# Performance work log

Measured on AMD Instinct MI355X. Metric: run time of the kernel, lower is better.

Reference implementation:

```python
import jax, jax.numpy as jnp
import numpy as np

N = 50000
TOPK = 32
IN_C = 128
OUT_C = 64
NEG_SLOPE = 0.2
BN_EPS = 1e-5


def setup_inputs() -> dict:
    key = jax.random.key(0)
    ks = jax.random.split(key, 8)
    x = jax.random.normal(ks[0], (N, IN_C), dtype=jnp.float32)
    embedding = jax.random.normal(ks[1], (N, OUT_C), dtype=jnp.float32)
    # edges: each node has TOPK incoming edges, no self loops
    tgt = jnp.repeat(jnp.arange(N, dtype=jnp.int64), TOPK)
    off = jax.random.randint(ks[2], (N * TOPK,), 1, N, dtype=jnp.int64)
    src = (tgt + off) % N
    edge_index = jnp.stack([src, tgt], axis=0)
    lin_w = jax.random.normal(ks[3], (OUT_C, IN_C), dtype=jnp.float32) * (1.0 / np.sqrt(IN_C))
    att_i = jax.random.normal(ks[4], (1, 1, OUT_C), dtype=jnp.float32) * 0.1
    att_j = jax.random.normal(ks[5], (1, 1, OUT_C), dtype=jnp.float32) * 0.1
    att_em_i = jax.random.normal(ks[6], (1, 1, OUT_C), dtype=jnp.float32) * 0.1
    att_em_j = jax.random.normal(ks[7], (1, 1, OUT_C), dtype=jnp.float32) * 0.1
    bias = jnp.zeros((OUT_C,), dtype=jnp.float32)
    bn_gamma = jnp.ones((OUT_C,), dtype=jnp.float32)
    bn_beta = jnp.zeros((OUT_C,), dtype=jnp.float32)
    return {"x": x, "embedding": embedding, "edge_index": edge_index,
            "lin_w": lin_w, "att_i": att_i, "att_j": att_j,
            "att_em_i": att_em_i, "att_em_j": att_em_j, "bias": bias,
            "bn_gamma": bn_gamma, "bn_beta": bn_beta}


def _gnn_forward(x, embedding, lin_w, att_i, att_j, att_em_i, att_em_j,
                 bias, bn_gamma, bn_beta, src, tgt):
    n = x.shape[0]
    # linear transform: [N, heads=1, OUT_C]
    x_lin = (x @ lin_w.T).reshape(n, 1, OUT_C)
    # gather per edge (self loops already appended to src/tgt)
    x_i = x_lin[tgt]                      # [Etot, 1, C]
    x_j = x_lin[src]                      # [Etot, 1, C]
    emb_i = embedding[tgt][:, None, :]    # [Etot, 1, C]
    emb_j = embedding[src][:, None, :]
    # attention logits, eq (6)-(8)
    alpha = ((x_i * att_i).sum(-1) + (emb_i * att_em_i).sum(-1)
             + (x_j * att_j).sum(-1) + (emb_j * att_em_j).sum(-1))  # [Etot, 1]
    alpha = jnp.where(alpha >= 0, alpha, NEG_SLOPE * alpha)
    # segment softmax over incoming edges of each target node
    m = jax.ops.segment_max(alpha, tgt, num_segments=n)
    m = jnp.where(jnp.isfinite(m), m, 0.0)
    e = jnp.exp(alpha - m[tgt])
    denom = jax.ops.segment_sum(e, tgt, num_segments=n)
    alpha = e / (denom[tgt] + 1e-16)      # [Etot, 1]
    # weighted scatter-add aggregation
    msg = x_j * alpha[:, :, None]         # [Etot, 1, C]
    out = jax.ops.segment_sum(msg, tgt, num_segments=n).reshape(n, OUT_C)
    out = out + bias
    # BatchNorm1d (training-mode batch stats, biased var) + ReLU
    mu = out.mean(axis=0)
    var = ((out - mu) ** 2).mean(axis=0)
    out = (out - mu) / jnp.sqrt(var + BN_EPS) * bn_gamma + bn_beta
    return jax.nn.relu(out)


def reference(x, embedding, edge_index, lin_w, att_i, att_j, att_em_i,
              att_em_j, bias, bn_gamma, bn_beta):
    n = x.shape[0]
    loops = jnp.arange(n, dtype=edge_index.dtype)
    src = jnp.concatenate([edge_index[0], loops])
    tgt = jnp.concatenate([edge_index[1], loops])
    return _gnn_forward(x, embedding, lin_w, att_i, att_j, att_em_i,
                        att_em_j, bias, bn_gamma, bn_beta, src, tgt)
```

## Files before the change

kernel.cpp:

```cpp
#include <hip/hip_runtime.h>

#define NN 50000
#define TOPK 32
#define IN_C 128
#define OUT_C 64
#define NEG_SLOPE 0.2f
#define BN_EPS 1e-5f

#define K1_BLOCKS (NN / 16)
#define K2_BLOCKS (NN / 8)

#define WS_XBF   0
#define WS_AI    (NN * 32)
#define WS_AJ    (WS_AI + NN)
#define WS_SUMS  (WS_AJ + NN)

typedef __bf16 bf16x8 __attribute__((ext_vector_type(8)));
typedef float f32x4 __attribute__((ext_vector_type(4)));
union BF8 { unsigned short u[8]; bf16x8 v; };

__device__ inline float leaky(float a) { return a >= 0.f ? a : NEG_SLOPE * a; }
__device__ inline float bl(unsigned u) { return __uint_as_float(u << 16); }
__device__ inline float bh(unsigned u) { return __uint_as_float(u & 0xffff0000u); }

__device__ inline unsigned short f2bf(float f) {
    unsigned u = __float_as_uint(f);
    unsigned r = (u + 0x7fffu + ((u >> 16) & 1u)) >> 16;
    return (unsigned short)r;
}

__device__ inline void async16(const uint4* g, uint4* l) {
    __builtin_amdgcn_global_load_lds(
        (const __attribute__((address_space(1))) void*)(const void*)g,
        (__attribute__((address_space(3))) void*)(void*)l, 16, 0, 0);
}

__global__ __launch_bounds__(256) void k1_mfma(
    const float* __restrict__ x, const float* __restrict__ emb,
    const float* __restrict__ lin_w,
    const float* __restrict__ att_i, const float* __restrict__ att_j,
    const float* __restrict__ att_em_i, const float* __restrict__ att_em_j,
    unsigned short* __restrict__ x_bf, float* __restrict__ a_i,
    float* __restrict__ a_j, float* __restrict__ sums)
{
    __shared__ float redi[16][5], redj[16][5];
    __shared__ float eredi[16][17], eredj[16][17];
    const int tid = threadIdx.x;
    if (blockIdx.x == 0) {
#pragma unroll
        for (int i = 0; i < 4; ++i) sums[tid + i * 256] = 0.f;
    }

    const int lane = tid & 63;
    const int wv = tid >> 6;
    const int quad = lane >> 4;
    const int nn = lane & 15;
    const int base = blockIdx.x * 16;
    const int c = wv * 16 + nn;

    BF8 bfr[4], afr[4];
    {
        const float* wr = lin_w + (size_t)c * IN_C + quad * 8;
        const float* xr = x + (size_t)(base + nn) * IN_C + quad * 8;
#pragma unroll
        for (int s = 0; s < 4; ++s) {
            const float4 wa = *(const float4*)(wr + s * 32);
            const float4 wb = *(const float4*)(wr + s * 32 + 4);
            const float4 xa = *(const float4*)(xr + s * 32);
            const float4 xb = *(const float4*)(xr + s * 32 + 4);
            bfr[s].u[0] = f2bf(wa.x); bfr[s].u[1] = f2bf(wa.y);
            bfr[s].u[2] = f2bf(wa.z); bfr[s].u[3] = f2bf(wa.w);
            bfr[s].u[4] = f2bf(wb.x); bfr[s].u[5] = f2bf(wb.y);
            bfr[s].u[6] = f2bf(wb.z); bfr[s].u[7] = f2bf(wb.w);
            afr[s].u[0] = f2bf(xa.x); afr[s].u[1] = f2bf(xa.y);
            afr[s].u[2] = f2bf(xa.z); afr[s].u[3] = f2bf(xa.w);
            afr[s].u[4] = f2bf(xb.x); afr[s].u[5] = f2bf(xb.y);
            afr[s].u[6] = f2bf(xb.z); afr[s].u[7] = f2bf(xb.w);
        }
    }

    f32x4 acc = {0.f, 0.f, 0.f, 0.f};
#pragma unroll
    for (int s = 0; s < 4; ++s)
        acc = __builtin_amdgcn_mfma_f32_16x16x32_bf16(afr[s].v, bfr[s].v, acc,
                                                      0, 0, 0);

    const float aic = att_i[c], ajc = att_j[c];
    float pi[4], pj[4];
#pragma unroll
    for (int r = 0; r < 4; ++r) {
        const int node = base + quad * 4 + r;
        x_bf[(size_t)node * OUT_C + c] = f2bf(acc[r]);
        pi[r] = acc[r] * aic;
        pj[r] = acc[r] * ajc;
    }
#pragma unroll
    for (int d = 1; d < 16; d <<= 1) {
#pragma unroll
        for (int r = 0; r < 4; ++r) {
            pi[r] += __shfl_xor(pi[r], d, 64);
            pj[r] += __shfl_xor(pj[r], d, 64);
        }
    }
    if (nn == 0) {
#pragma unroll
        for (int r = 0; r < 4; ++r) {
            redi[quad * 4 + r][wv] = pi[r];
            redj[quad * 4 + r][wv] = pj[r];
        }
    }
    {
        const int nl = tid >> 4, c4 = tid & 15;
        const float4 e4 = ((const float4*)emb)[(size_t)(base + nl) * 16 + c4];
        const float4 i4 = ((const float4*)att_em_i)[c4];
        const float4 j4 = ((const float4*)att_em_j)[c4];
        eredi[nl][c4] = e4.x * i4.x + e4.y * i4.y + e4.z * i4.z + e4.w * i4.w;
        eredj[nl][c4] = e4.x * j4.x + e4.y * j4.y + e4.z * j4.z + e4.w * j4.w;
    }
    __syncthreads();
    if (tid < 16) {
        float si = redi[tid][0] + redi[tid][1] + redi[tid][2] + redi[tid][3];
        float sj = redj[tid][0] + redj[tid][1] + redj[tid][2] + redj[tid][3];
#pragma unroll
        for (int r = 0; r < 16; ++r) { si += eredi[tid][r]; sj += eredj[tid][r]; }
        a_i[base + tid] = si;
        a_j[base + tid] = sj;
    }
}

__global__ __launch_bounds__(64) void k2_attn(
    const int* __restrict__ src, const uint4* __restrict__ x_bf4,
    const float* __restrict__ a_j, const float* __restrict__ a_i,
    const float* __restrict__ bias, float* __restrict__ out,
    float* __restrict__ sums)
{
    __shared__ uint4 stage[33 * 64];
    __shared__ float wbuf[8][36];
    __shared__ float sb1[64][9], sb2[64][9];

    const int tid = threadIdx.x;
    const int g = tid >> 3;
    const int q = tid & 7;
    const int t = blockIdx.x * 8 + g;

    const int4* sp4 = (const int4*)(src + (size_t)t * TOPK);
    int4 s4[8];
#pragma unroll
    for (int i = 0; i < 8; ++i) s4[i] = sp4[i];
    const int4 sq = sp4[q];

#pragma unroll
    for (int i = 0; i < 8; ++i) {
        async16(x_bf4 + ((size_t)s4[i].x * 8 + q), &stage[(i * 4 + 0) * 64]);
        async16(x_bf4 + ((size_t)s4[i].y * 8 + q), &stage[(i * 4 + 1) * 64]);
        async16(x_bf4 + ((size_t)s4[i].z * 8 + q), &stage[(i * 4 + 2) * 64]);
        async16(x_bf4 + ((size_t)s4[i].w * 8 + q), &stage[(i * 4 + 3) * 64]);
    }
    async16(x_bf4 + ((size_t)t * 8 + q), &stage[32 * 64]);

    const float ai_t = a_i[t];
    float l0 = leaky(ai_t + a_j[sq.x]);
    float l1 = leaky(ai_t + a_j[sq.y]);
    float l2 = leaky(ai_t + a_j[sq.z]);
    float l3 = leaky(ai_t + a_j[sq.w]);
    const float ls = leaky(ai_t + a_j[t]);
    float mx = fmaxf(fmaxf(l0, l1), fmaxf(l2, l3));
#pragma unroll
    for (int d = 1; d < 8; d <<= 1) mx = fmaxf(mx, __shfl_xor(mx, d, 64));
    mx = fmaxf(mx, ls);
    const float e0 = __expf(l0 - mx), e1 = __expf(l1 - mx);
    const float e2 = __expf(l2 - mx), e3 = __expf(l3 - mx);
    const float es = __expf(ls - mx);
    float den = (e0 + e1) + (e2 + e3);
#pragma unroll
    for (int d = 1; d < 8; d <<= 1) den += __shfl_xor(den, d, 64);
    den += es + 1e-16f;
    const float inv = 1.f / den;

    ((float4*)&wbuf[g][q * 4])[0] =
        make_float4(e0 * inv, e1 * inv, e2 * inv, e3 * inv);
    if (q == 0) wbuf[g][32] = es * inv;
    __syncthreads();

    float4 w4[8];
#pragma unroll
    for (int i = 0; i < 8; ++i) w4[i] = ((const float4*)wbuf[g])[i];
    const float wself = wbuf[g][32];

    __builtin_amdgcn_s_waitcnt(0x0F70);
    __syncthreads();

    float A[8];
#pragma unroll
    for (int j = 0; j < 8; ++j) A[j] = 0.f;
#pragma unroll
    for (int e = 0; e < 33; ++e) {
        const uint4 u = stage[e * 64 + tid];
        const float w = (e < 32) ? ((const float*)&w4[e >> 2])[e & 3] : wself;
        A[0] = fmaf(w, bl(u.x), A[0]); A[1] = fmaf(w, bh(u.x), A[1]);
        A[2] = fmaf(w, bl(u.y), A[2]); A[3] = fmaf(w, bh(u.y), A[3]);
        A[4] = fmaf(w, bl(u.z), A[4]); A[5] = fmaf(w, bh(u.z), A[5]);
        A[6] = fmaf(w, bl(u.w), A[6]); A[7] = fmaf(w, bh(u.w), A[7]);
    }
    const float4 b0 = ((const float4*)bias)[q * 2];
    const float4 b1 = ((const float4*)bias)[q * 2 + 1];
    float v[8];
    v[0] = A[0] + b0.x; v[1] = A[1] + b0.y; v[2] = A[2] + b0.z; v[3] = A[3] + b0.w;
    v[4] = A[4] + b1.x; v[5] = A[5] + b1.y; v[6] = A[6] + b1.z; v[7] = A[7] + b1.w;
    float4* o4 = (float4*)(out + (size_t)t * OUT_C + q * 8);
    o4[0] = make_float4(v[0], v[1], v[2], v[3]);
    o4[1] = make_float4(v[4], v[5], v[6], v[7]);

#pragma unroll
    for (int j = 0; j < 8; ++j) {
        sb1[q * 8 + j][g] = v[j];
        sb2[q * 8 + j][g] = v[j] * v[j];
    }
    __syncthreads();
    {
        float t1 = 0.f, t2 = 0.f;
#pragma unroll
        for (int r = 0; r < 8; ++r) { t1 += sb1[tid][r]; t2 += sb2[tid][r]; }
        float* rep = sums + (blockIdx.x & 7) * 128;
        atomicAdd(&rep[tid], t1);
        atomicAdd(&rep[64 + tid], t2);
    }
}

__global__ __launch_bounds__(256) void k4_bn(
    float* __restrict__ out, const float* __restrict__ sums,
    const float* __restrict__ gamma, const float* __restrict__ beta)
{
    __shared__ float s_sc[64], s_sh[64];
    const int tid = threadIdx.x;
    if (tid < 64) {
        float s1 = 0.f, s2 = 0.f;
#pragma unroll
        for (int r = 0; r < 8; ++r) {
            s1 += sums[r * 128 + tid];
            s2 += sums[r * 128 + 64 + tid];
        }
        const float mu = s1 / (float)NN;
        const float ex2 = s2 / (float)NN;
        const float var = fmaxf(ex2 - mu * mu, 0.f);
        const float sc = gamma[tid] / sqrtf(var + BN_EPS);
        s_sc[tid] = sc;
        s_sh[tid] = beta[tid] - mu * sc;
    }
    __syncthreads();
    const int total = NN * OUT_C / 4;
    float4* p = (float4*)out;
    for (int idx = blockIdx.x * 256 + tid; idx < total; idx += gridDim.x * 256) {
        float4 v = p[idx];
        const int c0 = (idx & 15) * 4;
        v.x = fmaxf(fmaf(v.x, s_sc[c0 + 0], s_sh[c0 + 0]), 0.f);
        v.y = fmaxf(fmaf(v.y, s_sc[c0 + 1], s_sh[c0 + 1]), 0.f);
        v.z = fmaxf(fmaf(v.z, s_sc[c0 + 2], s_sh[c0 + 2]), 0.f);
        v.w = fmaxf(fmaf(v.w, s_sc[c0 + 3], s_sh[c0 + 3]), 0.f);
        p[idx] = v;
    }
}

extern "C" void kernel_launch(void* const* d_in, const int* in_sizes, int n_in,
                              void* d_out, int out_size, void* d_ws, size_t ws_size,
                              hipStream_t stream) {
    const float* x        = (const float*)d_in[0];
    const float* emb      = (const float*)d_in[1];
    const int*   edge     = (const int*)d_in[2];
    const float* lin_w    = (const float*)d_in[3];
    const float* att_i    = (const float*)d_in[4];
    const float* att_j    = (const float*)d_in[5];
    const float* att_em_i = (const float*)d_in[6];
    const float* att_em_j = (const float*)d_in[7];
    const float* bias     = (const float*)d_in[8];
    const float* gamma    = (const float*)d_in[9];
    const float* beta     = (const float*)d_in[10];

    float* ws    = (float*)d_ws;
    unsigned short* x_bf = (unsigned short*)(ws + WS_XBF);
    float* a_i   = ws + WS_AI;
    float* a_j   = ws + WS_AJ;
    float* sums  = ws + WS_SUMS;
    float* out   = (float*)d_out;

    k1_mfma<<<K1_BLOCKS, 256, 0, stream>>>(x, emb, lin_w, att_i, att_j,
                                           att_em_i, att_em_j, x_bf, a_i, a_j, sums);
    k2_attn<<<K2_BLOCKS, 64, 0, stream>>>(edge, (const uint4*)x_bf, a_j, a_i,
                                          bias, out, sums);
    k4_bn<<<1024, 256, 0, stream>>>(out, sums, gamma, beta);
}
```

Before: 163.4 us.

## Fold attention vectors into weight-projected vectors and drop LDS reductions in k1

Adds a one-block pre-kernel that computes lin_w^T·att_i and lin_w^T·att_j, so each node's attention logit becomes a direct fp32 dot product with the input row instead of a reduction over the MFMA output. In k1 this removes the shared-memory reduction arrays, the 16-wide shuffle reductions and the __syncthreads; one wave computes the logits with two shuffles. It also switches the bf16 conversion to native casts, adds an extra tiny kernel launch, and slightly changes numerics because the logits no longer go through the bf16 GEMM.

```diff
diff --git a/kernel.cpp b/kernel.cpp
--- a/kernel.cpp
+++ b/kernel.cpp
@@ -14,10 +14,11 @@
 #define WS_AI    (NN * 32)
 #define WS_AJ    (WS_AI + NN)
 #define WS_SUMS  (WS_AJ + NN)
+#define WS_WI    (WS_SUMS + 1024)
+#define WS_WJ    (WS_WI + 128)
 
 typedef __bf16 bf16x8 __attribute__((ext_vector_type(8)));
 typedef float f32x4 __attribute__((ext_vector_type(4)));
-union BF8 { unsigned short u[8]; bf16x8 v; };
 
 __device__ inline float leaky(float a) { return a >= 0.f ? a : NEG_SLOPE * a; }
 __device__ inline float bl(unsigned u) { return __uint_as_float(u << 16); }
@@ -28,6 +29,15 @@
     unsigned r = (u + 0x7fffu + ((u >> 16) & 1u)) >> 16;
     return (unsigned short)r;
 }
+__device__ inline bf16x8 cvt8(const float4 a, const float4 b) {
+    bf16x8 r;
+    r[0] = (__bf16)a.x; r[1] = (__bf16)a.y; r[2] = (__bf16)a.z; r[3] = (__bf16)a.w;
+    r[4] = (__bf16)b.x; r[5] = (__bf16)b.y; r[6] = (__bf16)b.z; r[7] = (__bf16)b.w;
+    return r;
+}
+__device__ inline float dot4(const float4 a, const float4 b) {
+    return fmaf(a.x, b.x, fmaf(a.y, b.y, fmaf(a.z, b.z, a.w * b.w)));
+}
 
 __device__ inline void async16(const uint4* g, uint4* l) {
     __builtin_amdgcn_global_load_lds(
@@ -35,22 +45,34 @@
         (__attribute__((address_space(3))) void*)(void*)l, 16, 0, 0);
 }
 
+__global__ __launch_bounds__(128) void k0_pre(
+    const float* __restrict__ lin_w, const float* __restrict__ att_i,
+    const float* __restrict__ att_j, float* __restrict__ wi,
+    float* __restrict__ wj, float* __restrict__ sums)
+{
+    const int k = threadIdx.x;
+    float si = 0.f, sj = 0.f;
+#pragma unroll 8
+    for (int c = 0; c < OUT_C; ++c) {
+        const float w = lin_w[c * IN_C + k];
+        si = fmaf(w, att_i[c], si);
+        sj = fmaf(w, att_j[c], sj);
+    }
+    wi[k] = si;
+    wj[k] = sj;
+#pragma unroll
+    for (int i = 0; i < 8; ++i) sums[k + i * 128] = 0.f;
+}
+
 __global__ __launch_bounds__(256) void k1_mfma(
     const float* __restrict__ x, const float* __restrict__ emb,
     const float* __restrict__ lin_w,
-    const float* __restrict__ att_i, const float* __restrict__ att_j,
+    const float* __restrict__ wi, const float* __restrict__ wj,
     const float* __restrict__ att_em_i, const float* __restrict__ att_em_j,
     unsigned short* __restrict__ x_bf, float* __restrict__ a_i,
-    float* __restrict__ a_j, float* __restrict__ sums)
-{
-    __shared__ float redi[16][5], redj[16][5];
-    __shared__ float eredi[16][17], eredj[16][17];
+    float* __restrict__ a_j)
+{
     const int tid = threadIdx.x;
-    if (blockIdx.x == 0) {
-#pragma unroll
-        for (int i = 0; i < 4; ++i) sums[tid + i * 256] = 0.f;
-    }
-
     const int lane = tid & 63;
     const int wv = tid >> 6;
     const int quad = lane >> 4;
@@ -58,74 +80,57 @@
     const int base = blockIdx.x * 16;
     const int c = wv * 16 + nn;
 
-    BF8 bfr[4], afr[4];
-    {
-        const float* wr = lin_w + (size_t)c * IN_C + quad * 8;
-        const float* xr = x + (size_t)(base + nn) * IN_C + quad * 8;
+    const float* wr = lin_w + (size_t)c * IN_C + quad * 8;
+    bf16x8 bfr[4];
+#pragma unroll
+    for (int s = 0; s < 4; ++s)
+        bfr[s] = cvt8(*(const float4*)(wr + s * 32),
+                      *(const float4*)(wr + s * 32 + 4));
+
+    const float* xr = x + (size_t)(base + nn) * IN_C + quad * 8;
+    float4 xa[4], xb[4];
+#pragma unroll
+    for (int s = 0; s < 4; ++s) {
+        xa[s] = *(const float4*)(xr + s * 32);
+        xb[s] = *(const float4*)(xr + s * 32 + 4);
+    }
+    bf16x8 afr[4];
+#pragma unroll
+    for (int s = 0; s < 4; ++s) afr[s] = cvt8(xa[s], xb[s]);
+
+    f32x4 acc = {0.f, 0.f, 0.f, 0.f};
+#pragma unroll
+    for (int s = 0; s < 4; ++s)
+        acc = __builtin_amdgcn_mfma_f32_16x16x32_bf16(afr[s], bfr[s], acc,
+                                                      0, 0, 0);
+
+    if (wv == 0) {
+        const float* wik = wi + quad * 8;
+        const float* wjk = wj + quad * 8;
+        float pi = 0.f, pj = 0.f;
 #pragma unroll
         for (int s = 0; s < 4; ++s) {
-            const float4 wa = *(const float4*)(wr + s * 32);
-            const float4 wb = *(const float4*)(wr + s * 32 + 4);
-            const float4 xa = *(const float4*)(xr + s * 32);
-            const float4 xb = *(const float4*)(xr + s * 32 + 4);
-            bfr[s].u[0] = f2bf(wa.x); bfr[s].u[1] = f2bf(wa.y);
-            bfr[s].u[2] = f2bf(wa.z); bfr[s].u[3] = f2bf(wa.w);
-            bfr[s].u[4] = f2bf(wb.x); bfr[s].u[5] = f2bf(wb.y);
-            bfr[s].u[6] = f2bf(wb.z); bfr[s].u[7] = f2bf(wb.w);
-            afr[s].u[0] = f2bf(xa.x); afr[s].u[1] = f2bf(xa.y);
-            afr[s].u[2] = f2bf(xa.z); afr[s].u[3] = f2bf(xa.w);
-            afr[s].u[4] = f2bf(xb.x); afr[s].u[5] = f2bf(xb.y);
-            afr[s].u[6] = f2bf(xb.z); afr[s].u[7] = f2bf(xb.w);
+            pi += dot4(xa[s], *(const float4*)(wik + s * 32));
+            pi += dot4(xb[s], *(const float4*)(wik + s * 32 + 4));
+            pj += dot4(xa[s], *(const float4*)(wjk + s * 32));
+            pj += dot4(xb[s], *(const float4*)(wjk + s * 32 + 4));
         }
-    }
-
-    f32x4 acc = {0.f, 0.f, 0.f, 0.f};
-#pragma unroll
-    for (int s = 0; s < 4; ++s)
-        acc = __builtin_amdgcn_mfma_f32_16x16x32_bf16(afr[s].v, bfr[s].v, acc,
-                                                      0, 0, 0);
-
-    const float aic = att_i[c], ajc = att_j[c];
-    float pi[4], pj[4];
-#pragma unroll
-    for (int r = 0; r < 4; ++r) {
-        const int node = base + quad * 4 + r;
-        x_bf[(size_t)node * OUT_C + c] = f2bf(acc[r]);
-        pi[r] = acc[r] * aic;
-        pj[r] = acc[r] * ajc;
-    }
-#pragma unroll
-    for (int d = 1; d < 16; d <<= 1) {
-#pragma unroll
-        for (int r = 0; r < 4; ++r) {
-            pi[r] += __shfl_xor(pi[r], d, 64);
-            pj[r] += __shfl_xor(pj[r], d, 64);
+        const float4* er = (const float4*)(emb + (size_t)(base + nn) * OUT_C
+                                           + quad * 16);
+#pragma unroll
+        for (int i = 0; i < 4; ++i) {
+            const float4 e = er[i];
+            pi += dot4(e, ((const float4*)att_em_i)[quad * 4 + i]);
+            pj += dot4(e, ((const float4*)att_em_j)[quad * 4 + i]);
         }
-    }
-    if (nn == 0) {
-#pragma unroll
-        for (int r = 0; r < 4; ++r) {
-            redi[quad * 4 + r][wv] = pi[r];
-            redj[quad * 4 + r][wv] = pj[r];
-        }
-    }
-    {
-        const int nl = tid >> 4, c4 = tid & 15;
-        const float4 e4 = ((const float4*)emb)[(size_t)(base + nl) * 16 + c4];
-        const float4 i4 = ((const float4*)att_em_i)[c4];
-        const float4 j4 = ((const float4*)att_em_j)[c4];
-        eredi[nl][c4] = e4.x * i4.x + e4.y * i4.y + e4.z * i4.z + e4.w * i4.w;
-        eredj[nl][c4] = e4.x * j4.x + e4.y * j4.y + e4.z * j4.z + e4.w * j4.w;
-    }
-    __syncthreads();
-    if (tid < 16) {
-        float si = redi[tid][0] + redi[tid][1] + redi[tid][2] + redi[tid][3];
-        float sj = redj[tid][0] + redj[tid][1] + redj[tid][2] + redj[tid][3];
-#pragma unroll
-        for (int r = 0; r < 16; ++r) { si += eredi[tid][r]; sj += eredj[tid][r]; }
-        a_i[base + tid] = si;
-        a_j[base + tid] = sj;
-    }
+        pi += __shfl_xor(pi, 16, 64); pi += __shfl_xor(pi, 32, 64);
+        pj += __shfl_xor(pj, 16, 64); pj += __shfl_xor(pj, 32, 64);
+        if (quad == 0) { a_i[base + nn] = pi; a_j[base + nn] = pj; }
+    }
+
+#pragma unroll
+    for (int r = 0; r < 4; ++r)
+        x_bf[(size_t)(base + quad * 4 + r) * OUT_C + c] = f2bf(acc[r]);
 }
 
 __global__ __launch_bounds__(64) void k2_attn(
@@ -281,10 +286,13 @@
     float* a_i   = ws + WS_AI;
     float* a_j   = ws + WS_AJ;
     float* sums  = ws + WS_SUMS;
+    float* wi    = ws + WS_WI;
+    float* wj    = ws + WS_WJ;
     float* out   = (float*)d_out;
 
-    k1_mfma<<<K1_BLOCKS, 256, 0, stream>>>(x, emb, lin_w, att_i, att_j,
-                                           att_em_i, att_em_j, x_bf, a_i, a_j, sums);
+    k0_pre<<<1, 128, 0, stream>>>(lin_w, att_i, att_j, wi, wj, sums);
+    k1_mfma<<<K1_BLOCKS, 256, 0, stream>>>(x, emb, lin_w, wi, wj,
+                                           att_em_i, att_em_j, x_bf, a_i, a_j);
     k2_attn<<<K2_BLOCKS, 64, 0, stream>>>(edge, (const uint4*)x_bf, a_j, a_i,
                                           bias, out, sums);
     k4_bn<<<1024, 256, 0, stream>>>(out, sums, gamma, beta);
```

After: 168.4 us. 1.03x slower.
